# Optimization experiments

Hardware: AMD Instinct MI355X
Metric: run time of the kernel (lower is better)

Reference implementation:

```python
import jax, jax.numpy as jnp
import numpy as np

NUM_LAYERS = 7
EPS = 1e-5

def _cross_indices(query_len, key_len, cross_range):
    # off-diagonal band indices, seq_mask=False
    idx = [key_len * i + j for i in range(query_len) for j in range(key_len)
           if abs(i - j) <= cross_range and i != j]
    return np.asarray(idx, dtype=np.int32)

def _conv_stack(x, conv_w, conv_b, prelu_a):
    # x: [N, C, A, A]; conv (1,3) kernel, padding (0,1); residual each layer
    out = x
    for l in range(NUM_LAYERS):
        y = jax.lax.conv_general_dilated(
            out, conv_w[l], window_strides=(1, 1), padding=((0, 0), (1, 1)),
            dimension_numbers=("NCHW", "OIHW", "NCHW"))
        y = y + conv_b[l][None, :, None, None]
        a = prelu_a[l]
        y = jnp.where(y >= 0, y, a * y)  # PReLU (single shared slope)
        out = y + out
    return out

def reference(primitive_weights, conv_w, conv_b, prelu_a, bsz, cross_range, agent_num):
    C = primitive_weights.shape[0] // bsz
    QL = primitive_weights.shape[1] // agent_num
    KL = primitive_weights.shape[2] // agent_num
    A = agent_num
    # [bsz, C, QL, A, KL, A] -> swap (A, KL) -> [bsz, C, QL*KL, A, A]
    pw = primitive_weights.reshape(bsz, C, QL, A, KL, A).transpose(0, 1, 2, 4, 3, 5)
    pw = pw.reshape(bsz, C, QL * KL, A, A)
    idx = _cross_indices(QL, KL, cross_range)
    Nc = idx.shape[0]
    sel = pw[:, :, idx]  # [bsz, C, Nc, A, A]
    x = sel.transpose(0, 2, 1, 3, 4).reshape(bsz * Nc, C, A, A)
    conv_out = _conv_stack(x, conv_w, conv_b, prelu_a)
    sparse = jax.nn.relu(x - jax.nn.sigmoid(conv_out))
    self_mask = (1.0 - jnp.eye(A, dtype=sparse.dtype))[None, None]
    sparse = sparse * self_mask
    filled = sparse.reshape(bsz, Nc, C, A, A).transpose(0, 2, 1, 3, 4)
    updated = jnp.zeros_like(pw).at[:, :, idx].set(filled)
    updated = updated.reshape(bsz, C, QL, KL, A, A).transpose(0, 1, 2, 4, 3, 5)
    updated = updated.reshape(bsz * C, QL * A, KL * A)
    we = jnp.exp(updated) - 1.0
    return we / (jnp.sum(we, axis=-1, keepdims=True) + EPS)

def setup_inputs() -> dict:
    key = jax.random.key(0)
    k0, k1, k2, k3 = jax.random.split(key, 4)
    bsz, C, QL, KL, A = 8, 8, 128, 128, 8
    return {
        "primitive_weights": jax.random.normal(k0, (bsz * C, QL * A, KL * A), jnp.float32),
        "conv_w": jax.random.normal(k1, (NUM_LAYERS, C, C, 1, 3), jnp.float32) * 0.2,
        "conv_b": jax.random.normal(k2, (NUM_LAYERS, C), jnp.float32) * 0.1,
        "prelu_a": jnp.full((NUM_LAYERS,), 0.25, jnp.float32),
        "bsz": bsz,
        "cross_range": 2,
        "agent_num": A,
    }
```

## Files before the change

### kernel.cpp

```cpp
#include <hip/hip_runtime.h>
#include <math.h>

#define NL 7

__global__ __launch_bounds__(256) void fused_kernel(
    const float* __restrict__ pw,
    const float* __restrict__ conv_w,
    const float* __restrict__ conv_b,
    const float* __restrict__ prelu_a,
    float* __restrict__ out)
{
    __shared__ float wts[NL][8][8][3];
    __shared__ float bs[NL][8];
    __shared__ float al[NL];
    __shared__ float cur[4][8][64];
    __shared__ float rowinv[64];

    const int b = blockIdx.x >> 7;
    const int i = blockIdx.x & 127;
    const int t = threadIdx.x;
    const int dd = t >> 6;
    const int lane = t & 63;
    const int ai = lane >> 3, aj = lane & 7;
    const int dj = (dd < 2) ? dd - 2 : dd - 1;
    const int j = i + dj;
    const bool valid = (j >= 0) && (j < 128);

    for (int p = t; p < NL * 8 * 8 * 3; p += 256) ((float*)wts)[p] = conv_w[p];
    for (int p = t; p < NL * 8; p += 256)         ((float*)bs)[p]  = conv_b[p];
    if (t < NL) al[t] = prelu_a[t];

    float x[8], h[8];
    const float* base = pw + (((size_t)(b * 8)) << 20)
                           + (size_t)(i * 8 + ai) * 1024
                           + (size_t)((valid ? j : 0) * 8 + aj);
    #pragma unroll
    for (int c = 0; c < 8; ++c) {
        x[c] = valid ? base[((size_t)c) << 20] : 0.f;
        h[c] = x[c];
        cur[dd][c][lane] = x[c];
    }
    __syncthreads();

    for (int l = 0; l < NL; ++l) {
        float v0[8], v2[8];
        #pragma unroll
        for (int ci = 0; ci < 8; ++ci) {
            v0[ci] = (aj > 0) ? cur[dd][ci][lane - 1] : 0.f;
            v2[ci] = (aj < 7) ? cur[dd][ci][lane + 1] : 0.f;
        }
        const float a = al[l];
        float nxt[8];
        #pragma unroll
        for (int co = 0; co < 8; ++co) {
            float acc = bs[l][co];
            #pragma unroll
            for (int ci = 0; ci < 8; ++ci) {
                acc += wts[l][co][ci][0] * v0[ci]
                     + wts[l][co][ci][1] * h[ci]
                     + wts[l][co][ci][2] * v2[ci];
            }
            float y = (acc >= 0.f) ? acc : a * acc;
            nxt[co] = y + h[co];
        }
        __syncthreads();
        #pragma unroll
        for (int co = 0; co < 8; ++co) {
            h[co] = nxt[co];
            cur[dd][co][lane] = nxt[co];
        }
        __syncthreads();
    }

    #pragma unroll
    for (int c = 0; c < 8; ++c) {
        float sg = 1.f / (1.f + __expf(-h[c]));
        float s = x[c] - sg;
        s = (s > 0.f) ? s : 0.f;
        float we = (valid && ai != aj) ? expm1f(s) : 0.f;
        cur[dd][c][lane] = we;
    }
    __syncthreads();

    if (t < 64) {
        const int c = t >> 3, aii = t & 7;
        float s = 0.f;
        #pragma unroll
        for (int d2 = 0; d2 < 4; ++d2)
            #pragma unroll
            for (int a2 = 0; a2 < 8; ++a2)
                s += cur[d2][c][aii * 8 + a2];
        rowinv[t] = 1.f / (s + 1e-5f);
    }
    __syncthreads();

    const int row0 = t >> 6;
    const int l64  = t & 63;
    for (int g = 0; g < 16; ++g) {
        const int row = g * 4 + row0;
        const int c  = row >> 3;
        const int airow = row & 7;
        const float inv = rowinv[row];
        float4* rowp = (float4*)(out + ((((size_t)(b * 8 + c)) * 1024
                                         + (size_t)(i * 8 + airow)) << 10));
        #pragma unroll
        for (int k = 0; k < 4; ++k) {
            const int col4 = k * 64 + l64;
            const int jc = col4 >> 1;
            const int djc = jc - i;
            float4 v = make_float4(0.f, 0.f, 0.f, 0.f);
            if (djc >= -2 && djc <= 2 && djc != 0) {
                const int d2 = (djc < 0) ? djc + 2 : djc + 1;
                const int off = airow * 8 + (col4 & 1) * 4;
                v.x = cur[d2][c][off + 0] * inv;
                v.y = cur[d2][c][off + 1] * inv;
                v.z = cur[d2][c][off + 2] * inv;
                v.w = cur[d2][c][off + 3] * inv;
            }
            rowp[col4] = v;
        }
    }
}

extern "C" void kernel_launch(void* const* d_in, const int* in_sizes, int n_in,
                              void* d_out, int out_size, void* d_ws, size_t ws_size,
                              hipStream_t stream) {
    const float* pw      = (const float*)d_in[0];
    const float* conv_w  = (const float*)d_in[1];
    const float* conv_b  = (const float*)d_in[2];
    const float* prelu_a = (const float*)d_in[3];
    (void)d_ws; (void)ws_size;

    fused_kernel<<<8 * 128, 256, 0, stream>>>(pw, conv_w, conv_b, prelu_a,
                                              (float*)d_out);
}
```

Before: 413.2 us.

## Use wavefront shuffles for conv neighbors and split zero-fill into memset

The conv stack now exchanges neighbor columns with __shfl_up/__shfl_down on a 64-wide wavefront instead of shared memory, which removes two barriers per layer. The fused kernel no longer writes the full dense output rows. A hipMemsetAsync zeroes the whole output and the kernel writes only the band entries for valid j, using two float4 stores per row. The memset is a separate pass over the same 256MB output, so the cost depends on whether memset bandwidth beats the fused writes.

```diff
diff --git a/kernel.cpp b/kernel.cpp
--- a/kernel.cpp
+++ b/kernel.cpp
@@ -3,7 +3,7 @@
 
 #define NL 7
 
-__global__ __launch_bounds__(256) void fused_kernel(
+__global__ __launch_bounds__(256) void sparse_kernel(
     const float* __restrict__ pw,
     const float* __restrict__ conv_w,
     const float* __restrict__ conv_b,
@@ -13,7 +13,7 @@
     __shared__ float wts[NL][8][8][3];
     __shared__ float bs[NL][8];
     __shared__ float al[NL];
-    __shared__ float cur[4][8][64];
+    __shared__ float we_s[4][8][64];
     __shared__ float rowinv[64];
 
     const int b = blockIdx.x >> 7;
@@ -38,16 +38,18 @@
     for (int c = 0; c < 8; ++c) {
         x[c] = valid ? base[((size_t)c) << 20] : 0.f;
         h[c] = x[c];
-        cur[dd][c][lane] = x[c];
     }
+
     __syncthreads();
 
     for (int l = 0; l < NL; ++l) {
         float v0[8], v2[8];
         #pragma unroll
         for (int ci = 0; ci < 8; ++ci) {
-            v0[ci] = (aj > 0) ? cur[dd][ci][lane - 1] : 0.f;
-            v2[ci] = (aj < 7) ? cur[dd][ci][lane + 1] : 0.f;
+            float up = __shfl_up(h[ci], 1, 64);
+            float dn = __shfl_down(h[ci], 1, 64);
+            v0[ci] = (aj > 0) ? up : 0.f;
+            v2[ci] = (aj < 7) ? dn : 0.f;
         }
         const float a = al[l];
         float nxt[8];
@@ -63,13 +65,8 @@
             float y = (acc >= 0.f) ? acc : a * acc;
             nxt[co] = y + h[co];
         }
-        __syncthreads();
         #pragma unroll
-        for (int co = 0; co < 8; ++co) {
-            h[co] = nxt[co];
-            cur[dd][co][lane] = nxt[co];
-        }
-        __syncthreads();
+        for (int co = 0; co < 8; ++co) h[co] = nxt[co];
     }
 
     #pragma unroll
@@ -78,7 +75,7 @@
         float s = x[c] - sg;
         s = (s > 0.f) ? s : 0.f;
         float we = (valid && ai != aj) ? expm1f(s) : 0.f;
-        cur[dd][c][lane] = we;
+        we_s[dd][c][lane] = we;
     }
     __syncthreads();
 
@@ -89,36 +86,29 @@
         for (int d2 = 0; d2 < 4; ++d2)
             #pragma unroll
             for (int a2 = 0; a2 < 8; ++a2)
-                s += cur[d2][c][aii * 8 + a2];
+                s += we_s[d2][c][aii * 8 + a2];
         rowinv[t] = 1.f / (s + 1e-5f);
     }
     __syncthreads();
 
-    const int row0 = t >> 6;
-    const int l64  = t & 63;
-    for (int g = 0; g < 16; ++g) {
-        const int row = g * 4 + row0;
-        const int c  = row >> 3;
-        const int airow = row & 7;
+    if (valid) {
+        const int row = lane;
+        const int c = row >> 3, airow = row & 7;
         const float inv = rowinv[row];
-        float4* rowp = (float4*)(out + ((((size_t)(b * 8 + c)) * 1024
-                                         + (size_t)(i * 8 + airow)) << 10));
-        #pragma unroll
-        for (int k = 0; k < 4; ++k) {
-            const int col4 = k * 64 + l64;
-            const int jc = col4 >> 1;
-            const int djc = jc - i;
-            float4 v = make_float4(0.f, 0.f, 0.f, 0.f);
-            if (djc >= -2 && djc <= 2 && djc != 0) {
-                const int d2 = (djc < 0) ? djc + 2 : djc + 1;
-                const int off = airow * 8 + (col4 & 1) * 4;
-                v.x = cur[d2][c][off + 0] * inv;
-                v.y = cur[d2][c][off + 1] * inv;
-                v.z = cur[d2][c][off + 2] * inv;
-                v.w = cur[d2][c][off + 3] * inv;
-            }
-            rowp[col4] = v;
-        }
+        float4 lo, hi;
+        lo.x = we_s[dd][c][airow * 8 + 0] * inv;
+        lo.y = we_s[dd][c][airow * 8 + 1] * inv;
+        lo.z = we_s[dd][c][airow * 8 + 2] * inv;
+        lo.w = we_s[dd][c][airow * 8 + 3] * inv;
+        hi.x = we_s[dd][c][airow * 8 + 4] * inv;
+        hi.y = we_s[dd][c][airow * 8 + 5] * inv;
+        hi.z = we_s[dd][c][airow * 8 + 6] * inv;
+        hi.w = we_s[dd][c][airow * 8 + 7] * inv;
+        float4* p = (float4*)(out + (((size_t)(b * 8 + c)) << 20)
+                                  + (size_t)(i * 8 + airow) * 1024
+                                  + (size_t)j * 8);
+        p[0] = lo;
+        p[1] = hi;
     }
 }
 
@@ -131,6 +121,7 @@
     const float* prelu_a = (const float*)d_in[3];
     (void)d_ws; (void)ws_size;
 
-    fused_kernel<<<8 * 128, 256, 0, stream>>>(pw, conv_w, conv_b, prelu_a,
-                                              (float*)d_out);
+    hipMemsetAsync(d_out, 0, (size_t)out_size * sizeof(float), stream);
+    sparse_kernel<<<8 * 128, 256, 0, stream>>>(pw, conv_w, conv_b, prelu_a,
+                                               (float*)d_out);
 }
```

Measured after the change: 425.4 us. 2.9% more time.
